# Optimization experiments

Hardware: AMD Instinct MI355X
Metric: run time of the kernel (lower is better)

## Reference

```python
import jax, jax.numpy as jnp
import numpy as np

P = 64      # num_proxies
S = 4096    # num_samples
D = 128     # embed_dim
H = 2       # nhead
HD = D // H # head dim


def _edge_index():
    # dense bipartite edges: (p -> s) and (s -> p) for every proxy/sample pair
    p = np.arange(P)
    s = np.arange(S) + P
    pp = np.repeat(p, S)
    ss = np.tile(s, P)
    src = np.concatenate([pp, ss])
    dst = np.concatenate([ss, pp])
    return jnp.asarray(np.stack([src, dst]), dtype=jnp.int32)  # [2, 2*P*S]


def setup_inputs() -> dict:
    key = jax.random.key(0)
    ks = jax.random.split(key, 13)
    lin = lambda k, o, i: jax.random.normal(k, (o, i), dtype=jnp.float32) * (1.0 / np.sqrt(i))
    return {
        "x": jax.random.normal(ks[0], (S, D), dtype=jnp.float32),
        "proxies": jax.random.normal(ks[1], (P, D), dtype=jnp.float32),
        "Wq": lin(ks[2], D, D), "bq": jnp.zeros((D,), jnp.float32),
        "Wk": lin(ks[3], D, D), "bk": jnp.zeros((D,), jnp.float32),
        "Wv": lin(ks[4], D, D), "bv": jnp.zeros((D,), jnp.float32),
        "Wo": lin(ks[5], D, D), "bo": jnp.zeros((D,), jnp.float32),
        "Wfc": lin(ks[6], D, D), "bfc": jnp.zeros((D,), jnp.float32),
        "edge_index": _edge_index(),
    }


def reference(x, proxies, Wq, bq, Wk, bk, Wv, bv, Wo, bo, Wfc, bfc, edge_index):
    feats = jnp.concatenate([proxies, x], axis=0)  # [N, D], N = P + S
    N = feats.shape[0]
    q = (feats @ Wq.T + bq).reshape(N, H, HD)
    k = (feats @ Wk.T + bk).reshape(N, H, HD)
    v = (feats @ Wv.T + bv).reshape(N, H, HD)
    src, dst = edge_index[0], edge_index[1]
    # per-edge attention logits [E, H]
    scores = jnp.einsum('ehd,ehd->eh', q[dst], k[src]) / jnp.sqrt(jnp.float32(HD))
    # scatter-softmax over incoming edges of each target node
    smax = jax.ops.segment_max(scores, dst, num_segments=N)
    ex = jnp.exp(scores - smax[dst])
    denom = jax.ops.segment_sum(ex, dst, num_segments=N)
    alpha = ex / denom[dst]                                   # [E, H]
    agg = jax.ops.segment_sum(alpha[:, :, None] * v[src], dst, num_segments=N)  # [N, H, HD]
    h = agg.reshape(N, D) @ Wo.T + bo
    h = jax.nn.relu(h)  # nn.Dropout in eval mode = identity
    preds = h @ Wfc.T + bfc
    return preds[P:], h[P:]
```

## Files before the change

### kernel.cpp

```cpp
#include <hip/hip_runtime.h>
#include <hip/hip_bf16.h>

#define SS 4096
#define DD 128
#define PP 64
#define NH 2
#define HDIM 64

typedef unsigned short u16;
typedef __attribute__((ext_vector_type(8))) short short8;
typedef __attribute__((ext_vector_type(4))) float float4v;

__device__ inline float bf2f(u16 u) {
    union { unsigned int i; float f; } v; v.i = ((unsigned int)u) << 16; return v.f;
}
__device__ inline u16 f2bf(float f) {
    union { float f; unsigned int i; } v; v.f = f;
    unsigned int i = v.i;
    return (u16)((i + 0x7fffu + ((i >> 16) & 1u)) >> 16);
}

__device__ inline bool detect_f32(const void* raw) {
    const u16* w = (const u16*)raw;
    const int lane = threadIdx.x & 63;
    bool hit = false;
    #pragma unroll
    for (int j = 0; j < 4; ++j) {
        u16 x = w[lane * 4 + j];
        int e = (x >> 7) & 0xFF;
        hit |= (e >= 0xBF);
    }
    return __ballot(hit) != 0ull;
}

template<bool F32>
__device__ inline float lds1(const void* p, int idx) {
    if constexpr (F32) return ((const float*)p)[idx];
    else               return bf2f(((const u16*)p)[idx]);
}

template<bool F32>
__device__ inline short8 ld8(const void* p, int idx) {
    if constexpr (!F32) {
        return *(const short8*)((const u16*)p + idx);
    } else {
        const float* f = (const float*)p + idx;
        float4 a = *(const float4*)f;
        float4 b = *(const float4*)(f + 4);
        short8 r;
        r[0] = (short)f2bf(a.x); r[1] = (short)f2bf(a.y);
        r[2] = (short)f2bf(a.z); r[3] = (short)f2bf(a.w);
        r[4] = (short)f2bf(b.x); r[5] = (short)f2bf(b.y);
        r[6] = (short)f2bf(b.z); r[7] = (short)f2bf(b.w);
        return r;
    }
}

template<bool F32>
__device__ inline void st1(void* p, size_t idx, float v) {
    if constexpr (F32) ((float*)p)[idx] = v;
    else               ((u16*)p)[idx]   = f2bf(v);
}

template<bool F32>
__device__ void prep_kv_impl(
    const void* __restrict__ proxies,
    const void* __restrict__ Wk, const void* __restrict__ bk,
    const void* __restrict__ Wv, const void* __restrict__ bv,
    u16* __restrict__ Kp, u16* __restrict__ VT)
{
    __shared__ float pf[DD];
    const int p = blockIdx.x;
    const int t = threadIdx.x;
    pf[t] = lds1<F32>(proxies, p * DD + t);
    __syncthreads();
    float ak = 0.f, av = 0.f;
    for (int c = 0; c < DD / 8; ++c) {
        short8 wk = ld8<F32>(Wk, t * DD + c * 8);
        short8 wv = ld8<F32>(Wv, t * DD + c * 8);
        #pragma unroll
        for (int j = 0; j < 8; ++j) {
            float xv = pf[c * 8 + j];
            ak += xv * bf2f((u16)wk[j]);
            av += xv * bf2f((u16)wv[j]);
        }
    }
    ak += lds1<F32>(bk, t);
    av += lds1<F32>(bv, t);
    Kp[p * DD + t] = f2bf(ak);
    VT[t * PP + p] = f2bf(av);
}

__global__ __launch_bounds__(128) void prep_kv(
    const void* proxies, const void* Wk, const void* bk,
    const void* Wv, const void* bv, u16* Kp, u16* VT)
{
    if (detect_f32(proxies)) prep_kv_impl<true >(proxies, Wk, bk, Wv, bv, Kp, VT);
    else                     prep_kv_impl<false>(proxies, Wk, bk, Wv, bv, Kp, VT);
}

template<bool F32>
__device__ void fused_impl(
    const void* __restrict__ x,
    const void* __restrict__ Wq, const void* __restrict__ bq,
    const void* __restrict__ Wo, const void* __restrict__ bo,
    const void* __restrict__ Wfc, const void* __restrict__ bfc,
    const u16* __restrict__ Kp, const u16* __restrict__ VT,
    void* __restrict__ d_out)
{
    __shared__ __attribute__((aligned(16))) u16 q_lds[16][136];
    __shared__ __attribute__((aligned(16))) float sc_lds[NH][16][68];
    __shared__ __attribute__((aligned(16))) u16 al_lds[NH][16][72];
    __shared__ __attribute__((aligned(16))) u16 ag_lds[16][136];
    __shared__ __attribute__((aligned(16))) u16 h_lds[16][136];

    const int tid  = threadIdx.x;
    const int wave = tid >> 6;
    const int lane = tid & 63;
    const int lm   = lane & 15;
    const int quad = lane >> 4;
    const int s0   = blockIdx.x * 16;

    {
        float4v acc[2] = {{0,0,0,0},{0,0,0,0}};
        #pragma unroll
        for (int kt = 0; kt < 4; ++kt) {
            short8 a = ld8<F32>(x, (s0 + lm) * DD + kt * 32 + quad * 8);
            #pragma unroll
            for (int nt = 0; nt < 2; ++nt) {
                int d = (2 * wave + nt) * 16 + lm;
                short8 b = ld8<F32>(Wq, d * DD + kt * 32 + quad * 8);
                acc[nt] = __builtin_amdgcn_mfma_f32_16x16x32_bf16(a, b, acc[nt], 0, 0, 0);
            }
        }
        #pragma unroll
        for (int nt = 0; nt < 2; ++nt) {
            int col = (2 * wave + nt) * 16 + lm;
            float bias = lds1<F32>(bq, col);
            #pragma unroll
            for (int r = 0; r < 4; ++r)
                q_lds[quad * 4 + r][col] = f2bf(acc[nt][r] + bias);
        }
    }
    __syncthreads();

    const int head = wave >> 1;
    const int wh   = wave & 1;
    {
        float4v acc[2] = {{0,0,0,0},{0,0,0,0}};
        #pragma unroll
        for (int kt = 0; kt < 2; ++kt) {
            short8 a = *(const short8*)(&q_lds[lm][head * HDIM + kt * 32 + quad * 8]);
            #pragma unroll
            for (int nt = 0; nt < 2; ++nt) {
                int p = (wh * 2 + nt) * 16 + lm;
                short8 b = *(const short8*)(Kp + p * DD + head * HDIM + kt * 32 + quad * 8);
                acc[nt] = __builtin_amdgcn_mfma_f32_16x16x32_bf16(a, b, acc[nt], 0, 0, 0);
            }
        }
        const float scale = 0.125f;
        #pragma unroll
        for (int nt = 0; nt < 2; ++nt) {
            int p = (wh * 2 + nt) * 16 + lm;
            #pragma unroll
            for (int r = 0; r < 4; ++r)
                sc_lds[head][quad * 4 + r][p] = acc[nt][r] * scale;
        }
    }
    __syncthreads();

    if (tid < 32) {
        int s = tid & 15, hh = tid >> 4;
        float m = -1e30f;
        for (int p = 0; p < PP; ++p) m = fmaxf(m, sc_lds[hh][s][p]);
        float sum = 0.f;
        for (int p = 0; p < PP; ++p) {
            float e = __expf(sc_lds[hh][s][p] - m);
            sum += e;
            sc_lds[hh][s][p] = e;
        }
        float inv = 1.f / sum;
        for (int p = 0; p < PP; ++p)
            al_lds[hh][s][p] = f2bf(sc_lds[hh][s][p] * inv);
    }
    __syncthreads();

    {
        float4v acc[2] = {{0,0,0,0},{0,0,0,0}};
        #pragma unroll
        for (int kt = 0; kt < 2; ++kt) {
            short8 a = *(const short8*)(&al_lds[head][lm][kt * 32 + quad * 8]);
            #pragma unroll
            for (int nt = 0; nt < 2; ++nt) {
                int hd = (wh * 2 + nt) * 16 + lm;
                short8 b = *(const short8*)(VT + (head * HDIM + hd) * PP + kt * 32 + quad * 8);
                acc[nt] = __builtin_amdgcn_mfma_f32_16x16x32_bf16(a, b, acc[nt], 0, 0, 0);
            }
        }
        #pragma unroll
        for (int nt = 0; nt < 2; ++nt) {
            int col = head * HDIM + (wh * 2 + nt) * 16 + lm;
            #pragma unroll
            for (int r = 0; r < 4; ++r)
                ag_lds[quad * 4 + r][col] = f2bf(acc[nt][r]);
        }
    }
    __syncthreads();

    {
        float4v acc[2] = {{0,0,0,0},{0,0,0,0}};
        #pragma unroll
        for (int kt = 0; kt < 4; ++kt) {
            short8 a = *(const short8*)(&ag_lds[lm][kt * 32 + quad * 8]);
            #pragma unroll
            for (int nt = 0; nt < 2; ++nt) {
                int d = (2 * wave + nt) * 16 + lm;
                short8 b = ld8<F32>(Wo, d * DD + kt * 32 + quad * 8);
                acc[nt] = __builtin_amdgcn_mfma_f32_16x16x32_bf16(a, b, acc[nt], 0, 0, 0);
            }
        }
        #pragma unroll
        for (int nt = 0; nt < 2; ++nt) {
            int col = (2 * wave + nt) * 16 + lm;
            float bias = lds1<F32>(bo, col);
            #pragma unroll
            for (int r = 0; r < 4; ++r) {
                int row = quad * 4 + r;
                float hv = fmaxf(acc[nt][r] + bias, 0.f);
                h_lds[row][col] = f2bf(hv);
                st1<F32>(d_out, (size_t)SS * DD + (size_t)(s0 + row) * DD + col, hv);
            }
        }
    }
    __syncthreads();

    {
        float4v acc[2] = {{0,0,0,0},{0,0,0,0}};
        #pragma unroll
        for (int kt = 0; kt < 4; ++kt) {
            short8 a = *(const short8*)(&h_lds[lm][kt * 32 + quad * 8]);
            #pragma unroll
            for (int nt = 0; nt < 2; ++nt) {
                int d = (2 * wave + nt) * 16 + lm;
                short8 b = ld8<F32>(Wfc, d * DD + kt * 32 + quad * 8);
                acc[nt] = __builtin_amdgcn_mfma_f32_16x16x32_bf16(a, b, acc[nt], 0, 0, 0);
            }
        }
        #pragma unroll
        for (int nt = 0; nt < 2; ++nt) {
            int col = (2 * wave + nt) * 16 + lm;
            float bias = lds1<F32>(bfc, col);
            #pragma unroll
            for (int r = 0; r < 4; ++r) {
                int row = quad * 4 + r;
                st1<F32>(d_out, (size_t)(s0 + row) * DD + col, acc[nt][r] + bias);
            }
        }
    }
}

__global__ __launch_bounds__(256) void fused_gnn(
    const void* x,
    const void* Wq, const void* bq,
    const void* Wo, const void* bo,
    const void* Wfc, const void* bfc,
    const u16* Kp, const u16* VT,
    void* d_out)
{
    if (detect_f32(x)) fused_impl<true >(x, Wq, bq, Wo, bo, Wfc, bfc, Kp, VT, d_out);
    else               fused_impl<false>(x, Wq, bq, Wo, bo, Wfc, bfc, Kp, VT, d_out);
}

extern "C" void kernel_launch(void* const* d_in, const int* in_sizes, int n_in,
                              void* d_out, int out_size, void* d_ws, size_t ws_size,
                              hipStream_t stream) {
    const void* x    = d_in[0];
    const void* prox = d_in[1];
    const void* Wq   = d_in[2];
    const void* bq   = d_in[3];
    const void* Wk   = d_in[4];
    const void* bk   = d_in[5];
    const void* Wv   = d_in[6];
    const void* bv   = d_in[7];
    const void* Wo   = d_in[8];
    const void* bo   = d_in[9];
    const void* Wfc  = d_in[10];
    const void* bfc  = d_in[11];

    u16* Kp = (u16*)d_ws;
    u16* VT = Kp + PP * DD;

    prep_kv<<<PP, DD, 0, stream>>>(prox, Wk, bk, Wv, bv, Kp, VT);
    fused_gnn<<<SS / 16, 256, 0, stream>>>(x, Wq, bq, Wo, bo, Wfc, bfc,
                                           Kp, VT, d_out);
}
```

Before: 97.99 us.

## Fuse proxy K/V projection into main kernel and parallelize softmax

Drops the separate prep_kv launch. Each of the 256 blocks now recomputes the proxy K and V projections with MFMA into LDS and reads them from there in the score and aggregation steps. The softmax now uses 64 threads, each pair splitting a row and combining results with shuffles. This removes a kernel launch and its serial dependency, at the cost of redundant K/V work in every block and more LDS per block, which may lower occupancy.

```diff
diff --git a/kernel.cpp b/kernel.cpp
--- a/kernel.cpp
+++ b/kernel.cpp
@@ -63,56 +63,22 @@
 }
 
 template<bool F32>
-__device__ void prep_kv_impl(
-    const void* __restrict__ proxies,
-    const void* __restrict__ Wk, const void* __restrict__ bk,
-    const void* __restrict__ Wv, const void* __restrict__ bv,
-    u16* __restrict__ Kp, u16* __restrict__ VT)
-{
-    __shared__ float pf[DD];
-    const int p = blockIdx.x;
-    const int t = threadIdx.x;
-    pf[t] = lds1<F32>(proxies, p * DD + t);
-    __syncthreads();
-    float ak = 0.f, av = 0.f;
-    for (int c = 0; c < DD / 8; ++c) {
-        short8 wk = ld8<F32>(Wk, t * DD + c * 8);
-        short8 wv = ld8<F32>(Wv, t * DD + c * 8);
-        #pragma unroll
-        for (int j = 0; j < 8; ++j) {
-            float xv = pf[c * 8 + j];
-            ak += xv * bf2f((u16)wk[j]);
-            av += xv * bf2f((u16)wv[j]);
-        }
-    }
-    ak += lds1<F32>(bk, t);
-    av += lds1<F32>(bv, t);
-    Kp[p * DD + t] = f2bf(ak);
-    VT[t * PP + p] = f2bf(av);
-}
-
-__global__ __launch_bounds__(128) void prep_kv(
-    const void* proxies, const void* Wk, const void* bk,
-    const void* Wv, const void* bv, u16* Kp, u16* VT)
-{
-    if (detect_f32(proxies)) prep_kv_impl<true >(proxies, Wk, bk, Wv, bv, Kp, VT);
-    else                     prep_kv_impl<false>(proxies, Wk, bk, Wv, bv, Kp, VT);
-}
-
-template<bool F32>
 __device__ void fused_impl(
-    const void* __restrict__ x,
-    const void* __restrict__ Wq, const void* __restrict__ bq,
-    const void* __restrict__ Wo, const void* __restrict__ bo,
+    const void* __restrict__ x,    const void* __restrict__ proxies,
+    const void* __restrict__ Wq,  const void* __restrict__ bq,
+    const void* __restrict__ Wk,  const void* __restrict__ bk,
+    const void* __restrict__ Wv,  const void* __restrict__ bv,
+    const void* __restrict__ Wo,  const void* __restrict__ bo,
     const void* __restrict__ Wfc, const void* __restrict__ bfc,
-    const u16* __restrict__ Kp, const u16* __restrict__ VT,
     void* __restrict__ d_out)
 {
-    __shared__ __attribute__((aligned(16))) u16 q_lds[16][136];
+    __shared__ __attribute__((aligned(16))) u16   K_lds[PP][136];
+    __shared__ __attribute__((aligned(16))) u16   VT_lds[DD][72];
+    __shared__ __attribute__((aligned(16))) u16   q_lds[16][136];
     __shared__ __attribute__((aligned(16))) float sc_lds[NH][16][68];
-    __shared__ __attribute__((aligned(16))) u16 al_lds[NH][16][72];
-    __shared__ __attribute__((aligned(16))) u16 ag_lds[16][136];
-    __shared__ __attribute__((aligned(16))) u16 h_lds[16][136];
+    __shared__ __attribute__((aligned(16))) u16   al_lds[NH][16][72];
+    __shared__ __attribute__((aligned(16))) u16   ag_lds[16][136];
+    __shared__ __attribute__((aligned(16))) u16   h_lds[16][136];
 
     const int tid  = threadIdx.x;
     const int wave = tid >> 6;
@@ -122,6 +88,49 @@
     const int s0   = blockIdx.x * 16;
 
     {
+        float4v accK[4][2], accV[4][2];
+        #pragma unroll
+        for (int rt = 0; rt < 4; ++rt)
+            #pragma unroll
+            for (int ci = 0; ci < 2; ++ci) {
+                accK[rt][ci] = (float4v){0,0,0,0};
+                accV[rt][ci] = (float4v){0,0,0,0};
+            }
+        #pragma unroll
+        for (int kt = 0; kt < 4; ++kt) {
+            short8 a[4];
+            #pragma unroll
+            for (int rt = 0; rt < 4; ++rt)
+                a[rt] = ld8<F32>(proxies, (rt * 16 + lm) * DD + kt * 32 + quad * 8);
+            #pragma unroll
+            for (int ci = 0; ci < 2; ++ci) {
+                int d = (2 * wave + ci) * 16 + lm;
+                short8 bK = ld8<F32>(Wk, d * DD + kt * 32 + quad * 8);
+                short8 bV = ld8<F32>(Wv, d * DD + kt * 32 + quad * 8);
+                #pragma unroll
+                for (int rt = 0; rt < 4; ++rt) {
+                    accK[rt][ci] = __builtin_amdgcn_mfma_f32_16x16x32_bf16(a[rt], bK, accK[rt][ci], 0, 0, 0);
+                    accV[rt][ci] = __builtin_amdgcn_mfma_f32_16x16x32_bf16(a[rt], bV, accV[rt][ci], 0, 0, 0);
+                }
+            }
+        }
+        #pragma unroll
+        for (int ci = 0; ci < 2; ++ci) {
+            int d = (2 * wave + ci) * 16 + lm;
+            float bkv = lds1<F32>(bk, d);
+            float bvv = lds1<F32>(bv, d);
+            #pragma unroll
+            for (int rt = 0; rt < 4; ++rt)
+                #pragma unroll
+                for (int r = 0; r < 4; ++r) {
+                    int p = rt * 16 + quad * 4 + r;
+                    K_lds[p][d]  = f2bf(accK[rt][ci][r] + bkv);
+                    VT_lds[d][p] = f2bf(accV[rt][ci][r] + bvv);
+                }
+        }
+    }
+
+    {
         float4v acc[2] = {{0,0,0,0},{0,0,0,0}};
         #pragma unroll
         for (int kt = 0; kt < 4; ++kt) {
@@ -154,7 +163,7 @@
             #pragma unroll
             for (int nt = 0; nt < 2; ++nt) {
                 int p = (wh * 2 + nt) * 16 + lm;
-                short8 b = *(const short8*)(Kp + p * DD + head * HDIM + kt * 32 + quad * 8);
+                short8 b = *(const short8*)(&K_lds[p][head * HDIM + kt * 32 + quad * 8]);
                 acc[nt] = __builtin_amdgcn_mfma_f32_16x16x32_bf16(a, b, acc[nt], 0, 0, 0);
             }
         }
@@ -169,19 +178,24 @@
     }
     __syncthreads();
 
-    if (tid < 32) {
-        int s = tid & 15, hh = tid >> 4;
+    if (tid < 64) {
+        int s = tid & 15, hh = (tid >> 4) & 1, half = tid >> 5;
+        const float* row = &sc_lds[hh][s][0];
         float m = -1e30f;
-        for (int p = 0; p < PP; ++p) m = fmaxf(m, sc_lds[hh][s][p]);
-        float sum = 0.f;
-        for (int p = 0; p < PP; ++p) {
-            float e = __expf(sc_lds[hh][s][p] - m);
-            sum += e;
-            sc_lds[hh][s][p] = e;
-        }
+        #pragma unroll
+        for (int j = 0; j < 32; ++j) m = fmaxf(m, row[half * 32 + j]);
+        m = fmaxf(m, __shfl_xor(m, 32));
+        float e[32], sum = 0.f;
+        #pragma unroll
+        for (int j = 0; j < 32; ++j) {
+            e[j] = __expf(row[half * 32 + j] - m);
+            sum += e[j];
+        }
+        sum += __shfl_xor(sum, 32);
         float inv = 1.f / sum;
-        for (int p = 0; p < PP; ++p)
-            al_lds[hh][s][p] = f2bf(sc_lds[hh][s][p] * inv);
+        #pragma unroll
+        for (int j = 0; j < 32; ++j)
+            al_lds[hh][s][half * 32 + j] = f2bf(e[j] * inv);
     }
     __syncthreads();
 
@@ -193,7 +207,7 @@
             #pragma unroll
             for (int nt = 0; nt < 2; ++nt) {
                 int hd = (wh * 2 + nt) * 16 + lm;
-                short8 b = *(const short8*)(VT + (head * HDIM + hd) * PP + kt * 32 + quad * 8);
+                short8 b = *(const short8*)(&VT_lds[head * HDIM + hd][kt * 32 + quad * 8]);
                 acc[nt] = __builtin_amdgcn_mfma_f32_16x16x32_bf16(a, b, acc[nt], 0, 0, 0);
             }
         }
@@ -260,37 +274,24 @@
 }
 
 __global__ __launch_bounds__(256) void fused_gnn(
-    const void* x,
-    const void* Wq, const void* bq,
-    const void* Wo, const void* bo,
+    const void* x,   const void* proxies,
+    const void* Wq,  const void* bq,
+    const void* Wk,  const void* bk,
+    const void* Wv,  const void* bv,
+    const void* Wo,  const void* bo,
     const void* Wfc, const void* bfc,
-    const u16* Kp, const u16* VT,
     void* d_out)
 {
-    if (detect_f32(x)) fused_impl<true >(x, Wq, bq, Wo, bo, Wfc, bfc, Kp, VT, d_out);
-    else               fused_impl<false>(x, Wq, bq, Wo, bo, Wfc, bfc, Kp, VT, d_out);
+    if (detect_f32(x))
+        fused_impl<true >(x, proxies, Wq, bq, Wk, bk, Wv, bv, Wo, bo, Wfc, bfc, d_out);
+    else
+        fused_impl<false>(x, proxies, Wq, bq, Wk, bk, Wv, bv, Wo, bo, Wfc, bfc, d_out);
 }
 
 extern "C" void kernel_launch(void* const* d_in, const int* in_sizes, int n_in,
                               void* d_out, int out_size, void* d_ws, size_t ws_size,
                               hipStream_t stream) {
-    const void* x    = d_in[0];
-    const void* prox = d_in[1];
-    const void* Wq   = d_in[2];
-    const void* bq   = d_in[3];
-    const void* Wk   = d_in[4];
-    const void* bk   = d_in[5];
-    const void* Wv   = d_in[6];
-    const void* bv   = d_in[7];
-    const void* Wo   = d_in[8];
-    const void* bo   = d_in[9];
-    const void* Wfc  = d_in[10];
-    const void* bfc  = d_in[11];
-
-    u16* Kp = (u16*)d_ws;
-    u16* VT = Kp + PP * DD;
-
-    prep_kv<<<PP, DD, 0, stream>>>(prox, Wk, bk, Wv, bv, Kp, VT);
-    fused_gnn<<<SS / 16, 256, 0, stream>>>(x, Wq, bq, Wo, bo, Wfc, bfc,
-                                           Kp, VT, d_out);
-}
+    fused_gnn<<<SS / 16, 256, 0, stream>>>(
+        d_in[0], d_in[1], d_in[2], d_in[3], d_in[4], d_in[5], d_in[6],
+        d_in[7], d_in[8], d_in[9], d_in[10], d_in[11], d_out);
+}
```

Result: no change. 96.13 us (-1.9%).
